# Kernel tuning notes

Measured on AMD Instinct MI355X. Metric: run time of the kernel, lower is better.

Reference implementation:

```python
import jax, jax.numpy as jnp
import numpy as np

C, H, W, N = 256, 256, 256, 512
ROI_SIZE = 7


def setup_inputs() -> dict:
    key = jax.random.key(0)
    k1, k2, k3 = jax.random.split(key, 3)
    feature = jax.random.normal(k1, (C, H, W), dtype=jnp.float32)
    # rois layout: (y1, x1, y2, x2), valid boxes inside the map
    start = jax.random.uniform(k2, (N, 2), jnp.float32, 0.0, H / 2)
    size = jax.random.uniform(k3, (N, 2), jnp.float32, 8.0, H / 2)
    rois = jnp.concatenate([start, start + size], axis=-1)
    return {"feature": feature, "rois": rois}


def _bilinear(feature, x, y):
    # feature: [C, H, W]; x, y: [...] float sample coords.
    # Faithful to the torch code: corners are clamped BEFORE computing the
    # interpolation weights (y - y1, y2 - y, etc.).
    h, w = feature.shape[-2:]
    y1 = jnp.floor(y).astype(jnp.int32)
    y2 = y1 + 1
    x1 = jnp.floor(x).astype(jnp.int32)
    x2 = x1 + 1
    y1 = jnp.clip(y1, 0, h - 1)
    y2 = jnp.clip(y2, 0, h - 1)
    x1 = jnp.clip(x1, 0, w - 1)
    x2 = jnp.clip(x2, 0, w - 1)
    wy1 = y - y1  # dist to top (clamped) corner
    wy2 = y2 - y
    wx1 = x - x1
    wx2 = x2 - x
    f11 = feature[:, y1, x1]  # [C, ...]
    f12 = feature[:, y1, x2]
    f21 = feature[:, y2, x1]
    f22 = feature[:, y2, x2]
    p = f11 * wx2 + f12 * wx1
    q = f21 * wx2 + f22 * wx1
    return p * wy2 + q * wy1


def reference(feature, rois):
    # feature: [C, H, W]; rois: [N, 4] = (y1, x1, y2, x2)
    R = ROI_SIZE
    n_roi = rois.shape[0]
    c = feature.shape[0]
    stride_h = (rois[:, 2] - rois[:, 0]) / R  # [N]
    stride_w = (rois[:, 3] - rois[:, 1]) / R  # [N]
    bins = jnp.arange(R, dtype=feature.dtype)
    y_base = rois[:, 0, None] + stride_h[:, None] * bins  # [N, 7]
    x_base = rois[:, 1, None] + stride_w[:, None] * bins  # [N, 7]
    # two sample points per bin, at 1/3 and 2/3 of the bin stride
    ys = jnp.stack([y_base + stride_h[:, None] / 3,
                    y_base + 2 * stride_h[:, None] / 3], axis=-1)  # [N, 7, 2]
    xs = jnp.stack([x_base + stride_w[:, None] / 3,
                    x_base + 2 * stride_w[:, None] / 3], axis=-1)  # [N, 7, 2]
    # all (y_sample, x_sample) combos per (roi, bin_m, bin_n): [N, 7, 7, 2, 2]
    Y = ys[:, :, None, :, None]
    X = xs[:, None, :, None, :]
    Yb, Xb = jnp.broadcast_arrays(Y, X)
    vals = _bilinear(feature, Xb, Yb)  # [C, N, 7, 7, 2, 2]
    # Faithful to torch.max(cat(...)) on a [C, 4] tensor: a GLOBAL max over
    # both channels and the 4 sample points, broadcast back to all channels.
    pooled = vals.max(axis=(0, -2, -1))  # [N, 7, 7]
    return jnp.broadcast_to(pooled[:, None, :, :], (n_roi, c, R, R))
```

## Files before the change

### kernel.cpp

```cpp
#include <hip/hip_runtime.h>

#define CCH 256
#define HH  256
#define WW  256
#define HWSZ (HH * WW)
#define NROI 512
#define RBIN 7
#define NBIN (RBIN * RBIN)
#define TFEAT_BYTES ((size_t)HWSZ * CCH * 2)

typedef float vfloat4 __attribute__((ext_vector_type(4)));

__device__ __forceinline__ unsigned short f2bf_rne(float f) {
    unsigned u = __float_as_uint(f);
    u = (u + 0x7fffu + ((u >> 16) & 1u)) >> 16;
    return (unsigned short)u;
}

__global__ __launch_bounds__(256)
void transpose_chw_to_hwc_bf16(const float* __restrict__ feat,
                               unsigned short* __restrict__ tfeat)
{
    __shared__ __align__(16) float tile[64 * 64];
    const int t   = threadIdx.x;
    const int hw0 = blockIdx.x * 64;
    const int c0  = blockIdx.y * 64;

    const int cl_r = t >> 4;
    const int fc   = t & 15;

    vfloat4 v[4];
    #pragma unroll
    for (int j = 0; j < 4; ++j) {
        v[j] = __builtin_nontemporal_load(
            (const vfloat4*)(feat + (size_t)(c0 + cl_r + j * 16) * HWSZ + hw0 + 4 * fc));
    }
    #pragma unroll
    for (int j = 0; j < 4; ++j) {
        const int cl = cl_r + j * 16;
        const int p  = (4 * fc) ^ (4 * ((cl >> 2) & 7));
        *(vfloat4*)&tile[cl * 64 + p] = v[j];
    }
    __syncthreads();

    const int cl_w = (t & 15) * 4;
    const int swz  = 4 * ((t & 15) & 7);
    #pragma unroll
    for (int j = 0; j < 4; ++j) {
        const int hl = (t >> 4) + j * 16;
        const int pc = hl ^ swz;
        ushort4 w;
        w.x = f2bf_rne(tile[(cl_w + 0) * 64 + pc]);
        w.y = f2bf_rne(tile[(cl_w + 1) * 64 + pc]);
        w.z = f2bf_rne(tile[(cl_w + 2) * 64 + pc]);
        w.w = f2bf_rne(tile[(cl_w + 3) * 64 + pc]);
        *(ushort4*)(tfeat + (size_t)(hw0 + hl) * CCH + c0 + cl_w) = w;
    }
}

__global__ __launch_bounds__(1024)
void roialign_fused(const unsigned short* __restrict__ tfeat,
                    const float* __restrict__ rois,
                    float* __restrict__ out)
{
    const int n    = blockIdx.x;
    const int t    = threadIdx.x;
    const int wave = t >> 6;
    const int lane = t & 63;
    const int half = lane >> 5;
    const int cOff = (lane & 31) * 8;

    __shared__ float pooled[NBIN];

    const float y0 = rois[n * 4 + 0];
    const float x0 = rois[n * 4 + 1];
    const float sh = (rois[n * 4 + 2] - y0) / (float)RBIN;
    const float sw = (rois[n * 4 + 3] - x0) / (float)RBIN;

    for (int bin = wave; bin < NBIN; bin += 16) {
        const int by = bin / RBIN;
        const int bx = bin % RBIN;

        float acc[8];
        #pragma unroll
        for (int k = 0; k < 8; ++k) acc[k] = -INFINITY;

        #pragma unroll
        for (int i = 0; i < 2; ++i) {
            const int point = i * 2 + half;
            const int sy = point >> 1;
            const int sx = point & 1;

            const float y = y0 + sh * (float)by +
                            ((sy == 0) ? (sh / 3.0f) : (2.0f * sh / 3.0f));
            const float x = x0 + sw * (float)bx +
                            ((sx == 0) ? (sw / 3.0f) : (2.0f * sw / 3.0f));

            int iy1 = (int)floorf(y);
            int iy2 = iy1 + 1;
            int ix1 = (int)floorf(x);
            int ix2 = ix1 + 1;
            iy1 = min(max(iy1, 0), HH - 1);
            iy2 = min(max(iy2, 0), HH - 1);
            ix1 = min(max(ix1, 0), WW - 1);
            ix2 = min(max(ix2, 0), WW - 1);

            const float wy1 = y - (float)iy1;
            const float wy2 = (float)iy2 - y;
            const float wx1 = x - (float)ix1;
            const float wx2 = (float)ix2 - x;

            const uint4 A = *(const uint4*)(tfeat + (size_t)(iy1 * WW + ix1) * CCH + cOff);
            const uint4 B = *(const uint4*)(tfeat + (size_t)(iy1 * WW + ix2) * CCH + cOff);
            const uint4 C = *(const uint4*)(tfeat + (size_t)(iy2 * WW + ix1) * CCH + cOff);
            const uint4 D = *(const uint4*)(tfeat + (size_t)(iy2 * WW + ix2) * CCH + cOff);
            const unsigned* ap = (const unsigned*)&A;
            const unsigned* bp = (const unsigned*)&B;
            const unsigned* cp = (const unsigned*)&C;
            const unsigned* dp = (const unsigned*)&D;

            #pragma unroll
            for (int k = 0; k < 4; ++k) {
                const unsigned ua = ap[k], ub = bp[k], uc = cp[k], ud = dp[k];
                {
                    const float f11 = __uint_as_float(ua << 16);
                    const float f12 = __uint_as_float(ub << 16);
                    const float f21 = __uint_as_float(uc << 16);
                    const float f22 = __uint_as_float(ud << 16);
                    const float p = f11 * wx2 + f12 * wx1;
                    const float q = f21 * wx2 + f22 * wx1;
                    acc[2 * k] = fmaxf(acc[2 * k], p * wy2 + q * wy1);
                }
                {
                    const float f11 = __uint_as_float(ua & 0xffff0000u);
                    const float f12 = __uint_as_float(ub & 0xffff0000u);
                    const float f21 = __uint_as_float(uc & 0xffff0000u);
                    const float f22 = __uint_as_float(ud & 0xffff0000u);
                    const float p = f11 * wx2 + f12 * wx1;
                    const float q = f21 * wx2 + f22 * wx1;
                    acc[2 * k + 1] = fmaxf(acc[2 * k + 1], p * wy2 + q * wy1);
                }
            }
        }

        float m = fmaxf(fmaxf(fmaxf(acc[0], acc[1]), fmaxf(acc[2], acc[3])),
                        fmaxf(fmaxf(acc[4], acc[5]), fmaxf(acc[6], acc[7])));

        #pragma unroll
        for (int off = 32; off > 0; off >>= 1)
            m = fmaxf(m, __shfl_xor(m, off, 64));

        if (lane == 0) pooled[bin] = m;
    }
    __syncthreads();

    float* o = out + (size_t)n * (CCH * NBIN);
    #pragma unroll
    for (int k = 0; k < 13; ++k) {
        const int idx = t + k * 1024;
        if (idx < CCH * NBIN)
            __builtin_nontemporal_store(pooled[idx % NBIN], o + idx);
    }
}

__global__ __launch_bounds__(256)
void roialign_direct_kernel(const float* __restrict__ feat,
                            const float* __restrict__ rois,
                            float* __restrict__ out)
{
    const int n = blockIdx.x;
    const int t = threadIdx.x;
    __shared__ float ptmax[196];
    __shared__ float pooled[NBIN];

    const float y0  = rois[n * 4 + 0];
    const float x0  = rois[n * 4 + 1];
    const float sh  = (rois[n * 4 + 2] - y0) / (float)RBIN;
    const float sw  = (rois[n * 4 + 3] - x0) / (float)RBIN;

    const bool active = (t < 196);
    int off11 = 0, off12 = 0, off21 = 0, off22 = 0;
    float wx1 = 0.f, wx2 = 0.f, wy1 = 0.f, wy2 = 0.f;
    if (active) {
        const int py = t / 14, px = t % 14;
        const int by = py >> 1, sy = py & 1;
        const int bx = px >> 1, sx = px & 1;
        const float y = y0 + sh * (float)by + ((sy == 0) ? (sh / 3.0f) : (2.0f * sh / 3.0f));
        const float x = x0 + sw * (float)bx + ((sx == 0) ? (sw / 3.0f) : (2.0f * sw / 3.0f));
        int iy1 = (int)floorf(y), iy2 = iy1 + 1;
        int ix1 = (int)floorf(x), ix2 = ix1 + 1;
        iy1 = min(max(iy1, 0), HH - 1); iy2 = min(max(iy2, 0), HH - 1);
        ix1 = min(max(ix1, 0), WW - 1); ix2 = min(max(ix2, 0), WW - 1);
        wy1 = y - (float)iy1; wy2 = (float)iy2 - y;
        wx1 = x - (float)ix1; wx2 = (float)ix2 - x;
        off11 = iy1 * WW + ix1; off12 = iy1 * WW + ix2;
        off21 = iy2 * WW + ix1; off22 = iy2 * WW + ix2;
    }
    if (active) {
        float m = -INFINITY;
        const float* f = feat;
        #pragma unroll 4
        for (int c = 0; c < CCH; ++c) {
            const float p = f[off11] * wx2 + f[off12] * wx1;
            const float q = f[off21] * wx2 + f[off22] * wx1;
            m = fmaxf(m, p * wy2 + q * wy1);
            f += HWSZ;
        }
        ptmax[t] = m;
    }
    __syncthreads();
    if (t < NBIN) {
        const int by = t / RBIN, bx = t % RBIN;
        const int p00 = (2 * by) * 14 + 2 * bx;
        pooled[t] = fmaxf(fmaxf(ptmax[p00], ptmax[p00 + 1]),
                          fmaxf(ptmax[p00 + 14], ptmax[p00 + 15]));
    }
    __syncthreads();
    float* o = out + (size_t)n * (CCH * NBIN);
    for (int idx = t; idx < CCH * NBIN; idx += 256)
        o[idx] = pooled[idx % NBIN];
}

extern "C" void kernel_launch(void* const* d_in, const int* in_sizes, int n_in,
                              void* d_out, int out_size, void* d_ws, size_t ws_size,
                              hipStream_t stream)
{
    const float* feat = (const float*)d_in[0];
    const float* rois = (const float*)d_in[1];
    float* out = (float*)d_out;

    if (ws_size < TFEAT_BYTES) {
        roialign_direct_kernel<<<NROI, 256, 0, stream>>>(feat, rois, out);
        return;
    }

    unsigned short* tfeat = (unsigned short*)d_ws;

    dim3 tgrid(HWSZ / 64, CCH / 64);
    transpose_chw_to_hwc_bf16<<<tgrid, 256, 0, stream>>>(feat, tfeat);

    roialign_fused<<<NROI, 1024, 0, stream>>>(tfeat, rois, out);
}
```

Baseline: 130.9 us.

## Split ROI bins into half-tasks per wave and vectorize output stores

Each wave now handles one of two sample-point pairs per bin (98 tasks instead of 49 bins), so the 16 waves are load-balanced better and each task issues fewer loads serially. Partial maxima go to shared memory and are combined in a second pass. The output broadcast is written with float4 nontemporal stores instead of scalar stores, and launch bounds add a min-blocks hint. This costs an extra barrier and shared buffer.

Measured after the change: 131.4 us. No clear change (+0.4%).

```diff
diff --git a/kernel.cpp b/kernel.cpp
--- a/kernel.cpp
+++ b/kernel.cpp
@@ -7,6 +7,7 @@
 #define NROI 512
 #define RBIN 7
 #define NBIN (RBIN * RBIN)
+#define NTASK (2 * NBIN)
 #define TFEAT_BYTES ((size_t)HWSZ * CCH * 2)
 
 typedef float vfloat4 __attribute__((ext_vector_type(4)));
@@ -58,7 +59,7 @@
     }
 }
 
-__global__ __launch_bounds__(1024)
+__global__ __launch_bounds__(1024, 8)
 void roialign_fused(const unsigned short* __restrict__ tfeat,
                     const float* __restrict__ rois,
                     float* __restrict__ out)
@@ -70,96 +71,100 @@
     const int half = lane >> 5;
     const int cOff = (lane & 31) * 8;
 
+    __shared__ float tmax[NTASK];
     __shared__ float pooled[NBIN];
 
     const float y0 = rois[n * 4 + 0];
     const float x0 = rois[n * 4 + 1];
-    const float sh = (rois[n * 4 + 2] - y0) / (float)RBIN;
-    const float sw = (rois[n * 4 + 3] - x0) / (float)RBIN;
-
-    for (int bin = wave; bin < NBIN; bin += 16) {
-        const int by = bin / RBIN;
-        const int bx = bin % RBIN;
-
-        float acc[8];
+    const float sh = (rois[n * 4 + 2] - y0) * (1.0f / (float)RBIN);
+    const float sw = (rois[n * 4 + 3] - x0) * (1.0f / (float)RBIN);
+
+    for (int task = wave; task < NTASK; task += 16) {
+        const int bin = task >> 1;
+        const int i   = task & 1;
+        const int by  = bin / RBIN;
+        const int bx  = bin - by * RBIN;
+
+        const int point = i * 2 + half;
+        const int sy = point >> 1;
+        const int sx = point & 1;
+
+        const float y = y0 + sh * (float)by +
+                        ((sy == 0) ? (sh * (1.0f / 3.0f)) : (sh * (2.0f / 3.0f)));
+        const float x = x0 + sw * (float)bx +
+                        ((sx == 0) ? (sw * (1.0f / 3.0f)) : (sw * (2.0f / 3.0f)));
+
+        int iy1 = (int)floorf(y);
+        int iy2 = iy1 + 1;
+        int ix1 = (int)floorf(x);
+        int ix2 = ix1 + 1;
+        iy1 = min(max(iy1, 0), HH - 1);
+        iy2 = min(max(iy2, 0), HH - 1);
+        ix1 = min(max(ix1, 0), WW - 1);
+        ix2 = min(max(ix2, 0), WW - 1);
+
+        const float wy1 = y - (float)iy1;
+        const float wy2 = (float)iy2 - y;
+        const float wx1 = x - (float)ix1;
+        const float wx2 = (float)ix2 - x;
+
+        const uint4 A = *(const uint4*)(tfeat + (size_t)(iy1 * WW + ix1) * CCH + cOff);
+        const uint4 B = *(const uint4*)(tfeat + (size_t)(iy1 * WW + ix2) * CCH + cOff);
+        const uint4 C = *(const uint4*)(tfeat + (size_t)(iy2 * WW + ix1) * CCH + cOff);
+        const uint4 D = *(const uint4*)(tfeat + (size_t)(iy2 * WW + ix2) * CCH + cOff);
+        const unsigned* ap = (const unsigned*)&A;
+        const unsigned* bp = (const unsigned*)&B;
+        const unsigned* cp = (const unsigned*)&C;
+        const unsigned* dp = (const unsigned*)&D;
+
+        float m = -INFINITY;
         #pragma unroll
-        for (int k = 0; k < 8; ++k) acc[k] = -INFINITY;
-
-        #pragma unroll
-        for (int i = 0; i < 2; ++i) {
-            const int point = i * 2 + half;
-            const int sy = point >> 1;
-            const int sx = point & 1;
-
-            const float y = y0 + sh * (float)by +
-                            ((sy == 0) ? (sh / 3.0f) : (2.0f * sh / 3.0f));
-            const float x = x0 + sw * (float)bx +
-                            ((sx == 0) ? (sw / 3.0f) : (2.0f * sw / 3.0f));
-
-            int iy1 = (int)floorf(y);
-            int iy2 = iy1 + 1;
-            int ix1 = (int)floorf(x);
-            int ix2 = ix1 + 1;
-            iy1 = min(max(iy1, 0), HH - 1);
-            iy2 = min(max(iy2, 0), HH - 1);
-            ix1 = min(max(ix1, 0), WW - 1);
-            ix2 = min(max(ix2, 0), WW - 1);
-
-            const float wy1 = y - (float)iy1;
-            const float wy2 = (float)iy2 - y;
-            const float wx1 = x - (float)ix1;
-            const float wx2 = (float)ix2 - x;
-
-            const uint4 A = *(const uint4*)(tfeat + (size_t)(iy1 * WW + ix1) * CCH + cOff);
-            const uint4 B = *(const uint4*)(tfeat + (size_t)(iy1 * WW + ix2) * CCH + cOff);
-            const uint4 C = *(const uint4*)(tfeat + (size_t)(iy2 * WW + ix1) * CCH + cOff);
-            const uint4 D = *(const uint4*)(tfeat + (size_t)(iy2 * WW + ix2) * CCH + cOff);
-            const unsigned* ap = (const unsigned*)&A;
-            const unsigned* bp = (const unsigned*)&B;
-            const unsigned* cp = (const unsigned*)&C;
-            const unsigned* dp = (const unsigned*)&D;
-
-            #pragma unroll
-            for (int k = 0; k < 4; ++k) {
-                const unsigned ua = ap[k], ub = bp[k], uc = cp[k], ud = dp[k];
-                {
-                    const float f11 = __uint_as_float(ua << 16);
-                    const float f12 = __uint_as_float(ub << 16);
-                    const float f21 = __uint_as_float(uc << 16);
-                    const float f22 = __uint_as_float(ud << 16);
-                    const float p = f11 * wx2 + f12 * wx1;
-                    const float q = f21 * wx2 + f22 * wx1;
-                    acc[2 * k] = fmaxf(acc[2 * k], p * wy2 + q * wy1);
-                }
-                {
-                    const float f11 = __uint_as_float(ua & 0xffff0000u);
-                    const float f12 = __uint_as_float(ub & 0xffff0000u);
-                    const float f21 = __uint_as_float(uc & 0xffff0000u);
-                    const float f22 = __uint_as_float(ud & 0xffff0000u);
-                    const float p = f11 * wx2 + f12 * wx1;
-                    const float q = f21 * wx2 + f22 * wx1;
-                    acc[2 * k + 1] = fmaxf(acc[2 * k + 1], p * wy2 + q * wy1);
-                }
+        for (int k = 0; k < 4; ++k) {
+            const unsigned ua = ap[k], ub = bp[k], uc = cp[k], ud = dp[k];
+            {
+                const float f11 = __uint_as_float(ua << 16);
+                const float f12 = __uint_as_float(ub << 16);
+                const float f21 = __uint_as_float(uc << 16);
+                const float f22 = __uint_as_float(ud << 16);
+                const float p = f11 * wx2 + f12 * wx1;
+                const float q = f21 * wx2 + f22 * wx1;
+                m = fmaxf(m, p * wy2 + q * wy1);
+            }
+            {
+                const float f11 = __uint_as_float(ua & 0xffff0000u);
+                const float f12 = __uint_as_float(ub & 0xffff0000u);
+                const float f21 = __uint_as_float(uc & 0xffff0000u);
+                const float f22 = __uint_as_float(ud & 0xffff0000u);
+                const float p = f11 * wx2 + f12 * wx1;
+                const float q = f21 * wx2 + f22 * wx1;
+                m = fmaxf(m, p * wy2 + q * wy1);
             }
         }
-
-        float m = fmaxf(fmaxf(fmaxf(acc[0], acc[1]), fmaxf(acc[2], acc[3])),
-                        fmaxf(fmaxf(acc[4], acc[5]), fmaxf(acc[6], acc[7])));
 
         #pragma unroll
         for (int off = 32; off > 0; off >>= 1)
             m = fmaxf(m, __shfl_xor(m, off, 64));
 
-        if (lane == 0) pooled[bin] = m;
-    }
+        if (lane == 0) tmax[task] = m;
+    }
+    __syncthreads();
+
+    if (t < NBIN) pooled[t] = fmaxf(tmax[2 * t], tmax[2 * t + 1]);
     __syncthreads();
 
     float* o = out + (size_t)n * (CCH * NBIN);
     #pragma unroll
-    for (int k = 0; k < 13; ++k) {
-        const int idx = t + k * 1024;
-        if (idx < CCH * NBIN)
-            __builtin_nontemporal_store(pooled[idx % NBIN], o + idx);
+    for (int k = 0; k < 4; ++k) {
+        const int idx4 = t + k * 1024;
+        if (idx4 < (CCH * NBIN) / 4) {
+            int r = (idx4 * 4) % NBIN;
+            vfloat4 v;
+            v.x = pooled[r]; r = (r == NBIN - 1) ? 0 : r + 1;
+            v.y = pooled[r]; r = (r == NBIN - 1) ? 0 : r + 1;
+            v.z = pooled[r]; r = (r == NBIN - 1) ? 0 : r + 1;
+            v.w = pooled[r];
+            __builtin_nontemporal_store(v, (vfloat4*)o + idx4);
+        }
     }
 }
 
```
